# Performance work log

Hardware: AMD Instinct MI355X
Metric: run time of the kernel (lower is better)

## Reference

```python
import jax, jax.numpy as jnp
import numpy as np

NS, B, T, S, H, V, G = 30, 16, 8, 400, 400, 20000, 3


def setup_inputs() -> dict:
    key = jax.random.key(0)
    ks = jax.random.split(key, 16)
    f = lambda k, shp, s: jax.random.normal(k, shp, jnp.float32) * s
    return dict(
        encoded_hidden=f(ks[0], (B, H), 1.0),
        encoded_outputs=f(ks[1], (B, S, H), 1.0),
        slot_emb=f(ks[2], (NS, H), 0.1),
        emb=f(ks[3], (V, H), 0.1),
        W_ih=f(ks[4], (3 * H, H), 0.05),
        W_hh=f(ks[5], (3 * H, H), 0.05),
        b_ih=jnp.zeros((3 * H,), jnp.float32),
        b_hh=jnp.zeros((3 * H,), jnp.float32),
        W_ratio_w=f(ks[6], (1, 3 * H), 0.05),
        W_ratio_b=jnp.zeros((1,), jnp.float32),
        W_gate_w=f(ks[7], (G, H), 0.05),
        W_gate_b=jnp.zeros((G,), jnp.float32),
        story=jax.random.randint(ks[8], (B, S), 0, V),
        target=jax.random.randint(ks[9], (B, NS, T), 0, V),
        encoded_lens=jax.random.randint(ks[10], (B,), S // 2, S + 1).astype(jnp.int32),
    )


def reference(encoded_hidden, encoded_outputs, slot_emb, emb, W_ih, W_hh, b_ih, b_hh,
              W_ratio_w, W_ratio_b, W_gate_w, W_gate_b, story, target, encoded_lens):
    ns, h = slot_emb.shape
    b, s, _ = encoded_outputs.shape
    t = target.shape[2]
    v = emb.shape[0]
    bs = ns * b  # fused slot*batch decode rows (parallel_decode)

    enc_out = jnp.tile(encoded_outputs, (ns, 1, 1))            # [bs,S,H]
    story_r = jnp.tile(story, (ns, 1))                          # [bs,S]
    lens_r = jnp.tile(encoded_lens, (ns,))                      # [bs]
    mask = jnp.arange(s)[None, :] < lens_r[:, None]             # [bs,S]
    h0 = jnp.tile(encoded_hidden, (ns, 1))                      # [bs,H]
    x0 = jnp.broadcast_to(slot_emb[:, None, :], (ns, b, h)).reshape(bs, h)
    # teacher-forcing inputs, slot-major flatten like target[:, :, wi].T.flatten()
    tf_in = emb[jnp.transpose(target, (2, 1, 0)).reshape(t, bs)]  # [T,bs,H]
    row = jnp.arange(bs)[:, None]
    neg_inf = jnp.float32(-jnp.inf)

    def gru_cell(x, hid):
        gi = x @ W_ih.T + b_ih
        gh = hid @ W_hh.T + b_hh
        ir, iz, inn = jnp.split(gi, 3, axis=-1)
        hr, hz, hn = jnp.split(gh, 3, axis=-1)
        r = jax.nn.sigmoid(ir + hr)
        z = jax.nn.sigmoid(iz + hz)
        n = jnp.tanh(inn + r * hn)
        return (1.0 - z) * n + z * hid

    def step(carry, x_next):
        hid, x = carry
        h_new = gru_cell(x, hid)                                # dec_state == hidden for 1-step GRU
        scores = jnp.einsum('bh,bsh->bs', h_new, enc_out)
        scores = jnp.where(mask, scores, neg_inf)
        prob = jax.nn.softmax(scores, axis=1)
        context = jnp.einsum('bs,bsh->bh', prob, enc_out)
        p_vocab = jax.nn.softmax(h_new @ emb.T, axis=1)         # [bs,V]
        p_gen_vec = jnp.concatenate([h_new, context, x], axis=-1)
        switch = jax.nn.sigmoid(p_gen_vec @ W_ratio_w.T + W_ratio_b)  # [bs,1]
        p_ctx = jnp.zeros((bs, v), p_vocab.dtype).at[row, story_r].add(prob)
        final = (1.0 - switch) * p_ctx + switch * p_vocab
        gate = context @ W_gate_w.T + W_gate_b
        return (h_new, x_next), (final, gate)

    _, (finals, gates) = jax.lax.scan(step, (h0, x0), tf_in)
    all_point = finals.reshape(t, ns, b, v).transpose(1, 2, 0, 3)  # [NS,B,T,V]
    all_gate = gates[0].reshape(ns, b, -1)                          # gates from wi==0
    return all_point, all_gate
```

## Files before the change

kernel.cpp:

```cpp
#include <hip/hip_runtime.h>
#include <hip/hip_bf16.h>

#define NSLOT 30
#define BB    16
#define TT    8
#define SS    400
#define HH    400
#define KP    416
#define NKK   13
#define VV    20000
#define GG    3
#define BSR   480
#define NBN   157
#define NCT   1256
#define FRAG_STRIDE 512

typedef __attribute__((ext_vector_type(8))) short bf16x8;
typedef __attribute__((ext_vector_type(4))) float f32x4;

__device__ __forceinline__ short f2bfs(float f){
  __hip_bfloat16 h = __float2bfloat16(f);
  union { __hip_bfloat16 b; short u; } v; v.b = h; return v.u;
}
__device__ __forceinline__ float sigm(float x){ return 1.f / (1.f + __expf(-x)); }
__device__ __forceinline__ float tanh_fast(float x){
  float e = __expf(2.f * x);
  return 1.f - 2.f / (e + 1.f);
}
__device__ __forceinline__ float wred_max(float v){
  #pragma unroll
  for (int off = 32; off; off >>= 1) v = fmaxf(v, __shfl_xor(v, off, 64));
  return v;
}
__device__ __forceinline__ float wred_sum(float v){
  #pragma unroll
  for (int off = 32; off; off >>= 1) v += __shfl_xor(v, off, 64);
  return v;
}

__global__ __launch_bounds__(256) void k_init(const float* __restrict__ eh,
                                              const float* __restrict__ semb,
                                              float* __restrict__ h_ws,
                                              float* __restrict__ x_ws)
{
  int idx = blockIdx.x * 256 + threadIdx.x;
  if (idx >= BSR * HH) return;
  int r = idx / HH, k = idx - r * HH;
  int batch = r % BB, slot = r / BB;
  h_ws[idx] = eh[batch * HH + k];
  x_ws[idx] = semb[slot * HH + k];
}

__global__ __launch_bounds__(256) void k_cast_emb(const float* __restrict__ emb,
                                                  short* __restrict__ ebf)
{
  const int nunit = NCT * NKK * 64;
  for (int u = blockIdx.x * 256 + threadIdx.x; u < nunit; u += gridDim.x * 256){
    int lane = u & 63;
    int kt = u >> 6;
    int ctile = kt / NKK, kk = kt - ctile * NKK;
    int lg = lane >> 4, cl = lane & 15;
    int c = ctile * 16 + cl;
    int k = kk * 32 + lg * 8;
    bf16x8 o;
    if (c < VV && k < HH){
      const float* src = emb + (size_t)c * HH + k;
      #pragma unroll
      for (int j = 0; j < 8; ++j) o[j] = f2bfs(src[j]);
    } else {
      #pragma unroll
      for (int j = 0; j < 8; ++j) o[j] = 0;
    }
    *reinterpret_cast<bf16x8*>(ebf + (size_t)u * 8) = o;
  }
}

__device__ __forceinline__ void gemm_acc(const float* __restrict__ A,
                                         const float* __restrict__ W,
                                         int N, int v0, int row0, int t,
                                         float acc[4][4])
{
  __shared__ float Af[64][36];
  __shared__ float Bf[64][132];
  const int cidx = t & 31, ridx = t >> 5;
  const int c0 = cidx * 4, r0 = ridx * 4;

  for (int kc = 0; kc < HH; kc += 64){
    const int Kc = (HH - kc >= 64) ? 64 : (HH - kc);
    const int sh = (Kc == 64) ? 4 : 2;
    {
      const int nunit = 32 << sh;
      for (int u = t; u < nunit; u += 256){
        int r = u >> sh;
        int k = (u & ((1 << sh) - 1)) << 2;
        float4 a4 = *reinterpret_cast<const float4*>(A + (size_t)(row0 + r) * HH + kc + k);
        Af[k][r] = a4.x; Af[k+1][r] = a4.y; Af[k+2][r] = a4.z; Af[k+3][r] = a4.w;
      }
    }
    {
      const int nunit = 128 << sh;
      for (int u = t; u < nunit; u += 256){
        int c = u >> sh;
        int k = (u & ((1 << sh) - 1)) << 2;
        float f0 = 0.f, f1 = 0.f, f2 = 0.f, f3 = 0.f;
        int col = v0 + c;
        if (col < N){
          float4 e = *reinterpret_cast<const float4*>(W + (size_t)col * HH + kc + k);
          f0 = e.x; f1 = e.y; f2 = e.z; f3 = e.w;
        }
        Bf[k][c] = f0; Bf[k+1][c] = f1; Bf[k+2][c] = f2; Bf[k+3][c] = f3;
      }
    }
    __syncthreads();
    #pragma unroll 8
    for (int k = 0; k < Kc; ++k){
      float4 a = *reinterpret_cast<const float4*>(&Af[k][r0]);
      float4 b = *reinterpret_cast<const float4*>(&Bf[k][c0]);
      acc[0][0] += a.x*b.x; acc[0][1] += a.x*b.y; acc[0][2] += a.x*b.z; acc[0][3] += a.x*b.w;
      acc[1][0] += a.y*b.x; acc[1][1] += a.y*b.y; acc[1][2] += a.y*b.z; acc[1][3] += a.y*b.w;
      acc[2][0] += a.z*b.x; acc[2][1] += a.z*b.y; acc[2][2] += a.z*b.z; acc[2][3] += a.z*b.w;
      acc[3][0] += a.w*b.x; acc[3][1] += a.w*b.y; acc[3][2] += a.w*b.z; acc[3][3] += a.w*b.w;
    }
    __syncthreads();
  }
}

__global__ __launch_bounds__(256) void k_gemm2(const float* __restrict__ x,
                                               const float* __restrict__ h,
                                               const float* __restrict__ Wih,
                                               const float* __restrict__ Whh,
                                               float* __restrict__ gi,
                                               float* __restrict__ gh, int nb1)
{
  const float* A; const float* W; float* C;
  int bx = blockIdx.x;
  if (bx < nb1){ A = x; W = Wih; C = gi; }
  else         { A = h; W = Whh; C = gh; bx -= nb1; }
  const int N = 3 * HH, v0 = bx * 128, row0 = blockIdx.y * 32, t = threadIdx.x;
  float acc[4][4] = {{0.f}};
  gemm_acc(A, W, N, v0, row0, t, acc);
  const int c0 = (t & 31) * 4, r0 = (t >> 5) * 4;
  #pragma unroll
  for (int i = 0; i < 4; ++i){
    int rr = row0 + r0 + i;
    #pragma unroll
    for (int j = 0; j < 4; ++j){
      int col = v0 + c0 + j;
      if (col < N) C[(size_t)rr * N + col] = acc[i][j];
    }
  }
}

__global__ __launch_bounds__(256) void k_logits_mfma(
    const short* __restrict__ hbf, const short* __restrict__ ebf,
    float* __restrict__ out, float* __restrict__ pmax_ws,
    float* __restrict__ psum_ws, int wi)
{
  const int t = threadIdx.x;
  const int lane = t & 63, wid = t >> 6;
  const int wr = wid >> 1, wc = wid & 1;
  const int l15 = lane & 15, lg = lane >> 4;
  const int bM = blockIdx.x, bN = blockIdx.y;

  const short* ap[2];
  const short* bp[4];
  #pragma unroll
  for (int m = 0; m < 2; ++m){
    int rtile = bM * 4 + wr * 2 + m;
    ap[m] = hbf + (size_t)min(rtile, BSR / 16 - 1) * (NKK * FRAG_STRIDE) + lane * 8;
  }
  #pragma unroll
  for (int n = 0; n < 4; ++n){
    int ctile = bN * 8 + wc * 4 + n;
    bp[n] = ebf + (size_t)ctile * (NKK * FRAG_STRIDE) + lane * 8;
  }

  f32x4 acc[2][4];
  #pragma unroll
  for (int m = 0; m < 2; ++m)
    #pragma unroll
    for (int n = 0; n < 4; ++n)
      acc[m][n] = (f32x4){0.f, 0.f, 0.f, 0.f};

  #pragma unroll
  for (int kk = 0; kk < NKK; ++kk){
    const int ko = kk * FRAG_STRIDE;
    bf16x8 a0 = *reinterpret_cast<const bf16x8*>(ap[0] + ko);
    bf16x8 a1 = *reinterpret_cast<const bf16x8*>(ap[1] + ko);
    #pragma unroll
    for (int n = 0; n < 4; ++n){
      bf16x8 b = *reinterpret_cast<const bf16x8*>(bp[n] + ko);
      acc[0][n] = __builtin_amdgcn_mfma_f32_16x16x32_bf16(a0, b, acc[0][n], 0, 0, 0);
      acc[1][n] = __builtin_amdgcn_mfma_f32_16x16x32_bf16(a1, b, acc[1][n], 0, 0, 0);
    }
  }

  #pragma unroll
  for (int m = 0; m < 2; ++m){
    #pragma unroll
    for (int q = 0; q < 4; ++q){
      int row = bM * 64 + wr * 32 + m * 16 + lg * 4 + q;
      if (row < BSR){
        float* orow = out + ((size_t)row * TT + wi) * VV;
        #pragma unroll
        for (int n = 0; n < 4; ++n){
          int col = bN * 128 + wc * 64 + n * 16 + l15;
          if (col < VV) orow[col] = acc[m][n][q];
        }
      }
    }
    f32x4 rmax, rsum;
    #pragma unroll
    for (int q = 0; q < 4; ++q){
      float mx = -3.0e38f;
      #pragma unroll
      for (int n = 0; n < 4; ++n){
        int col = bN * 128 + wc * 64 + n * 16 + l15;
        float v = (col < VV) ? acc[m][n][q] : -3.0e38f;
        mx = fmaxf(mx, v);
      }
      #pragma unroll
      for (int off = 1; off < 16; off <<= 1) mx = fmaxf(mx, __shfl_xor(mx, off, 64));
      float sm = 0.f;
      #pragma unroll
      for (int n = 0; n < 4; ++n){
        int col = bN * 128 + wc * 64 + n * 16 + l15;
        if (col < VV) sm += __expf(acc[m][n][q] - mx);
      }
      #pragma unroll
      for (int off = 1; off < 16; off <<= 1) sm += __shfl_xor(sm, off, 64);
      rmax[q] = mx; rsum[q] = sm;
    }
    if (l15 == 0){
      #pragma unroll
      for (int q = 0; q < 4; ++q){
        int row = bM * 64 + wr * 32 + m * 16 + lg * 4 + q;
        if (row < BSR){
          size_t pidx = ((size_t)row * NBN + bN) * 2 + wc;
          pmax_ws[pidx] = rmax[q];
          psum_ws[pidx] = rsum[q];
        }
      }
    }
  }
}

__global__ __launch_bounds__(256) void k_att(
    const float* __restrict__ enc, const float* __restrict__ emb,
    const float* __restrict__ b_ih, const float* __restrict__ b_hh,
    const float* __restrict__ Wr_w, const float* __restrict__ Wr_b,
    const float* __restrict__ Wg_w, const float* __restrict__ Wg_b,
    const int* __restrict__ target, const int* __restrict__ lens,
    const float* __restrict__ gi_ws, const float* __restrict__ gh_ws,
    float* __restrict__ h_ws, float* __restrict__ x_ws,
    short* __restrict__ h_bf,
    float* __restrict__ prob_ws, float* __restrict__ sw_ws,
    float* __restrict__ d_out, int wi)
{
  __shared__ float hn_s[HH];
  __shared__ float sc_s[SS];
  __shared__ float ctx_s[HH];
  __shared__ float red[4];
  __shared__ float redg[GG][4];

  const int t = threadIdx.x;
  const int rg = blockIdx.x;
  const int batch = rg % BB, slot = rg / BB;
  const int len = lens[batch];

  const float* gir = gi_ws + (size_t)rg * (3 * HH);
  const float* ghr = gh_ws + (size_t)rg * (3 * HH);
  for (int k = t; k < HH; k += 256){
    float irv = gir[k]          + b_ih[k];
    float izv = gir[HH + k]     + b_ih[HH + k];
    float inv = gir[2 * HH + k] + b_ih[2 * HH + k];
    float hrv = ghr[k]          + b_hh[k];
    float hzv = ghr[HH + k]     + b_hh[HH + k];
    float hnv = ghr[2 * HH + k] + b_hh[2 * HH + k];
    float rr = sigm(irv + hrv);
    float zz = sigm(izv + hzv);
    float nn = tanh_fast(inv + rr * hnv);
    float hold = h_ws[(size_t)rg * HH + k];
    float hnew = (1.f - zz) * nn + zz * hold;
    hn_s[k] = hnew;
    h_ws[(size_t)rg * HH + k] = hnew;
  }
  __syncthreads();

  if (t < KP / 8){
    const int kk = t >> 2, lg = t & 3;
    const int rtile = rg >> 4, rl = rg & 15;
    bf16x8 o;
    #pragma unroll
    for (int j = 0; j < 8; ++j){
      int k = t * 8 + j;
      o[j] = (k < HH) ? f2bfs(hn_s[k]) : (short)0;
    }
    *reinterpret_cast<bf16x8*>(
        h_bf + ((size_t)rtile * NKK + kk) * FRAG_STRIDE + (lg * 16 + rl) * 8) = o;
  }

  const float* encb = enc + (size_t)batch * SS * HH;
  float lmax = -3.0e38f;
  for (int s = t; s < SS; s += 256){
    if (s < len){
      const float4* er4 = reinterpret_cast<const float4*>(encb + (size_t)s * HH);
      float dot = 0.f;
      for (int k4 = 0; k4 < HH / 4; ++k4){
        float4 e = er4[k4];
        float4 hv = *reinterpret_cast<const float4*>(&hn_s[k4 * 4]);
        dot += e.x*hv.x + e.y*hv.y + e.z*hv.z + e.w*hv.w;
      }
      sc_s[s] = dot;
      lmax = fmaxf(lmax, dot);
    }
  }
  lmax = wred_max(lmax);
  if ((t & 63) == 0) red[t >> 6] = lmax;
  __syncthreads();
  lmax = fmaxf(fmaxf(red[0], red[1]), fmaxf(red[2], red[3]));
  float lsum = 0.f;
  for (int s = t; s < SS; s += 256){
    float e = (s < len) ? __expf(sc_s[s] - lmax) : 0.f;
    sc_s[s] = e;
    lsum += e;
  }
  lsum = wred_sum(lsum);
  __syncthreads();
  if ((t & 63) == 0) red[t >> 6] = lsum;
  __syncthreads();
  lsum = red[0] + red[1] + red[2] + red[3];
  float invl = 1.f / lsum;
  for (int s = t; s < SS; s += 256){
    float p = sc_s[s] * invl;
    sc_s[s] = p;
    prob_ws[(size_t)rg * SS + s] = p;
  }
  __syncthreads();

  for (int k = t; k < HH; k += 256){
    float c = 0.f;
    for (int s = 0; s < len; ++s)
      c += sc_s[s] * encb[(size_t)s * HH + k];
    ctx_s[k] = c;
  }
  __syncthreads();

  float sa = 0.f;
  for (int k = t; k < HH; k += 256){
    sa += Wr_w[k]          * hn_s[k]
        + Wr_w[HH + k]     * ctx_s[k]
        + Wr_w[2 * HH + k] * x_ws[(size_t)rg * HH + k];
  }
  sa = wred_sum(sa);
  if ((t & 63) == 0) red[t >> 6] = sa;
  __syncthreads();
  sa = red[0] + red[1] + red[2] + red[3];
  if (t == 0) sw_ws[rg] = sigm(sa + Wr_b[0]);

  if (wi == 0){
    float ga[GG] = {0.f, 0.f, 0.f};
    for (int k = t; k < HH; k += 256){
      float cv = ctx_s[k];
      ga[0] += Wg_w[k] * cv;
      ga[1] += Wg_w[HH + k] * cv;
      ga[2] += Wg_w[2 * HH + k] * cv;
    }
    #pragma unroll
    for (int g = 0; g < GG; ++g){
      ga[g] = wred_sum(ga[g]);
      if ((t & 63) == 0) redg[g][t >> 6] = ga[g];
    }
    __syncthreads();
    if (t < GG)
      d_out[(size_t)NSLOT * BB * TT * VV + (size_t)rg * GG + t] =
          redg[t][0] + redg[t][1] + redg[t][2] + redg[t][3] + Wg_b[t];
  }

  const int tgt = target[batch * (NSLOT * TT) + slot * TT + wi];
  const float* embrow = emb + (size_t)tgt * HH;
  for (int k = t; k < HH; k += 256)
    x_ws[(size_t)rg * HH + k] = embrow[k];
}

__global__ __launch_bounds__(256) void k_finalize(
    float* __restrict__ logits_out, const float* __restrict__ prob_ws,
    const float* __restrict__ pmax_ws, const float* __restrict__ psum_ws,
    const float* __restrict__ sw_ws, const int* __restrict__ story,
    const int* __restrict__ lens, int wi)
{
  __shared__ float pctx[VV];
  __shared__ float red[4];
  const int t = threadIdx.x;
  const int r = blockIdx.x;
  const int batch = r % BB;
  for (int v = t; v < VV; v += 256) pctx[v] = 0.f;
  __syncthreads();
  const int len = lens[batch];
  for (int s = t; s < SS; s += 256){
    if (s < len)
      atomicAdd(&pctx[story[batch * SS + s]], prob_ws[(size_t)r * SS + s]);
  }

  const float* pm = pmax_ws + (size_t)r * (NBN * 2);
  const float* ps = psum_ws + (size_t)r * (NBN * 2);
  float m = -3.0e38f;
  for (int i = t; i < NBN * 2; i += 256) m = fmaxf(m, pm[i]);
  m = wred_max(m);
  if ((t & 63) == 0) red[t >> 6] = m;
  __syncthreads();
  m = fmaxf(fmaxf(red[0], red[1]), fmaxf(red[2], red[3]));
  float lsum = 0.f;
  for (int i = t; i < NBN * 2; i += 256) lsum += ps[i] * __expf(pm[i] - m);
  lsum = wred_sum(lsum);
  __syncthreads();
  if ((t & 63) == 0) red[t >> 6] = lsum;
  __syncthreads();
  lsum = red[0] + red[1] + red[2] + red[3];

  const float sw = sw_ws[r];
  const float invl = sw / lsum;
  const float osw = 1.f - sw;
  float* lrow = logits_out + ((size_t)r * TT + wi) * VV;
  const float4* l4 = reinterpret_cast<const float4*>(lrow);
  float4* o4 = reinterpret_cast<float4*>(lrow);
  for (int i = t; i < VV / 4; i += 256){
    float4 q = l4[i];
    int v = i * 4;
    float4 o;
    o.x = __expf(q.x - m) * invl + osw * pctx[v + 0];
    o.y = __expf(q.y - m) * invl + osw * pctx[v + 1];
    o.z = __expf(q.z - m) * invl + osw * pctx[v + 2];
    o.w = __expf(q.w - m) * invl + osw * pctx[v + 3];
    o4[i] = o;
  }
}

extern "C" void kernel_launch(void* const* d_in, const int* in_sizes, int n_in,
                              void* d_out, int out_size, void* d_ws, size_t ws_size,
                              hipStream_t stream)
{
  (void)in_sizes; (void)n_in; (void)out_size; (void)ws_size;
  const float* eh    = (const float*)d_in[0];
  const float* enc   = (const float*)d_in[1];
  const float* semb  = (const float*)d_in[2];
  const float* emb   = (const float*)d_in[3];
  const float* W_ih  = (const float*)d_in[4];
  const float* W_hh  = (const float*)d_in[5];
  const float* b_ih  = (const float*)d_in[6];
  const float* b_hh  = (const float*)d_in[7];
  const float* Wr_w  = (const float*)d_in[8];
  const float* Wr_b  = (const float*)d_in[9];
  const float* Wg_w  = (const float*)d_in[10];
  const float* Wg_b  = (const float*)d_in[11];
  const int* story = (const int*)d_in[12];
  const int* tgt   = (const int*)d_in[13];
  const int* lens  = (const int*)d_in[14];
  float* out = (float*)d_out;

  float* ws      = (float*)d_ws;
  float* h_ws    = ws;
  float* x_ws    = ws + 192000;
  float* prob_ws = ws + 384000;
  float* sw_ws   = ws + 576000;
  float* gi_ws   = ws + 576512;
  float* gh_ws   = ws + 1152512;
  float* pmax_ws = ws + 1728512;
  float* psum_ws = ws + 1879552;
  short* h_bf    = (short*)(ws + 2030592);
  short* emb_bf  = (short*)(ws + 2130432);

  k_cast_emb<<<2048, 256, 0, stream>>>(emb, emb_bf);
  k_init<<<750, 256, 0, stream>>>(eh, semb, h_ws, x_ws);
  for (int wi = 0; wi < TT; ++wi){
    dim3 gg(20, 15);
    k_gemm2<<<gg, 256, 0, stream>>>(x_ws, h_ws, W_ih, W_hh, gi_ws, gh_ws, 10);
    k_att<<<BSR, 256, 0, stream>>>(enc, emb, b_ih, b_hh, Wr_w, Wr_b, Wg_w, Wg_b,
                                   tgt, lens, gi_ws, gh_ws, h_ws, x_ws, h_bf,
                                   prob_ws, sw_ws, out, wi);
    dim3 gl(8, NBN);
    k_logits_mfma<<<gl, 256, 0, stream>>>(h_bf, emb_bf, out, pmax_ws, psum_ws, wi);
    k_finalize<<<BSR, 256, 0, stream>>>(out, prob_ws, pmax_ws, psum_ws,
                                        sw_ws, story, lens, wi);
  }
}
```

Baseline: 1.178 ms.

## Store logits as packed bf16 in output row and enlarge MFMA M tile

The logits kernel now writes bf16 logits packed two per 32-bit word into the first half of each output row, halving the logit write and the finalize read traffic. Finalize first copies the bf16 row into shared memory so it can then overwrite the same row in place with fp32 probabilities. Each logits block also now computes four 16-row M tiles per wave instead of two, halving the grid in M and reusing each B fragment across more MFMAs at the cost of more accumulator registers. Rounding logits to bf16 before the exp adds small numerical error to the vocabulary probabilities.

Result: faster. 1.144 ms (-2.9%).

```diff
diff --git a/kernel.cpp b/kernel.cpp
--- a/kernel.cpp
+++ b/kernel.cpp
@@ -15,12 +15,19 @@
 #define NCT   1256
 #define FRAG_STRIDE 512
 
+typedef unsigned short u16;
 typedef __attribute__((ext_vector_type(8))) short bf16x8;
 typedef __attribute__((ext_vector_type(4))) float f32x4;
 
 __device__ __forceinline__ short f2bfs(float f){
   __hip_bfloat16 h = __float2bfloat16(f);
   union { __hip_bfloat16 b; short u; } v; v.b = h; return v.u;
+}
+__device__ __forceinline__ unsigned int pack2(float lo, float hi){
+  return (unsigned int)(u16)f2bfs(lo) | ((unsigned int)(u16)f2bfs(hi) << 16);
+}
+__device__ __forceinline__ float bfu(u16 u){
+  union { unsigned int i; float f; } v; v.i = ((unsigned int)u) << 16; return v.f;
 }
 __device__ __forceinline__ float sigm(float x){ return 1.f / (1.f + __expf(-x)); }
 __device__ __forceinline__ float tanh_fast(float x){
@@ -162,11 +169,11 @@
   const int l15 = lane & 15, lg = lane >> 4;
   const int bM = blockIdx.x, bN = blockIdx.y;
 
-  const short* ap[2];
+  const short* ap[4];
   const short* bp[4];
   #pragma unroll
-  for (int m = 0; m < 2; ++m){
-    int rtile = bM * 4 + wr * 2 + m;
+  for (int m = 0; m < 4; ++m){
+    int rtile = bM * 8 + wr * 4 + m;
     ap[m] = hbf + (size_t)min(rtile, BSR / 16 - 1) * (NKK * FRAG_STRIDE) + lane * 8;
   }
   #pragma unroll
@@ -175,9 +182,9 @@
     bp[n] = ebf + (size_t)ctile * (NKK * FRAG_STRIDE) + lane * 8;
   }
 
-  f32x4 acc[2][4];
-  #pragma unroll
-  for (int m = 0; m < 2; ++m)
+  f32x4 acc[4][4];
+  #pragma unroll
+  for (int m = 0; m < 4; ++m)
     #pragma unroll
     for (int n = 0; n < 4; ++n)
       acc[m][n] = (f32x4){0.f, 0.f, 0.f, 0.f};
@@ -185,28 +192,32 @@
   #pragma unroll
   for (int kk = 0; kk < NKK; ++kk){
     const int ko = kk * FRAG_STRIDE;
-    bf16x8 a0 = *reinterpret_cast<const bf16x8*>(ap[0] + ko);
-    bf16x8 a1 = *reinterpret_cast<const bf16x8*>(ap[1] + ko);
+    bf16x8 a[4];
+    #pragma unroll
+    for (int m = 0; m < 4; ++m)
+      a[m] = *reinterpret_cast<const bf16x8*>(ap[m] + ko);
     #pragma unroll
     for (int n = 0; n < 4; ++n){
       bf16x8 b = *reinterpret_cast<const bf16x8*>(bp[n] + ko);
-      acc[0][n] = __builtin_amdgcn_mfma_f32_16x16x32_bf16(a0, b, acc[0][n], 0, 0, 0);
-      acc[1][n] = __builtin_amdgcn_mfma_f32_16x16x32_bf16(a1, b, acc[1][n], 0, 0, 0);
-    }
-  }
-
-  #pragma unroll
-  for (int m = 0; m < 2; ++m){
+      #pragma unroll
+      for (int m = 0; m < 4; ++m)
+        acc[m][n] = __builtin_amdgcn_mfma_f32_16x16x32_bf16(a[m], b, acc[m][n], 0, 0, 0);
+    }
+  }
+
+  #pragma unroll
+  for (int m = 0; m < 4; ++m){
     #pragma unroll
     for (int q = 0; q < 4; ++q){
-      int row = bM * 64 + wr * 32 + m * 16 + lg * 4 + q;
-      if (row < BSR){
-        float* orow = out + ((size_t)row * TT + wi) * VV;
-        #pragma unroll
-        for (int n = 0; n < 4; ++n){
-          int col = bN * 128 + wc * 64 + n * 16 + l15;
-          if (col < VV) orow[col] = acc[m][n][q];
-        }
+      int row = bM * 128 + wr * 64 + m * 16 + lg * 4 + q;
+      u16* lrow16 = reinterpret_cast<u16*>(out + ((size_t)row * TT + wi) * VV);
+      #pragma unroll
+      for (int n = 0; n < 4; ++n){
+        float v = acc[m][n][q];
+        float vp = __shfl_xor(v, 1, 64);
+        int col = bN * 128 + wc * 64 + n * 16 + l15;
+        if (((l15 & 1) == 0) && row < BSR && col < VV)
+          *reinterpret_cast<unsigned int*>(lrow16 + col) = pack2(v, vp);
       }
     }
     f32x4 rmax, rsum;
@@ -234,7 +245,7 @@
     if (l15 == 0){
       #pragma unroll
       for (int q = 0; q < 4; ++q){
-        int row = bM * 64 + wr * 32 + m * 16 + lg * 4 + q;
+        int row = bM * 128 + wr * 64 + m * 16 + lg * 4 + q;
         if (row < BSR){
           size_t pidx = ((size_t)row * NBN + bN) * 2 + wc;
           pmax_ws[pidx] = rmax[q];
@@ -390,6 +401,7 @@
     const int* __restrict__ lens, int wi)
 {
   __shared__ float pctx[VV];
+  __shared__ u16 rowbuf[VV];
   __shared__ float red[4];
   const int t = threadIdx.x;
   const int r = blockIdx.x;
@@ -401,6 +413,11 @@
     if (s < len)
       atomicAdd(&pctx[story[batch * SS + s]], prob_ws[(size_t)r * SS + s]);
   }
+
+  float* lrow = logits_out + ((size_t)r * TT + wi) * VV;
+  const uint4* l16 = reinterpret_cast<const uint4*>(lrow);
+  for (int i = t; i < VV / 8; i += 256)
+    reinterpret_cast<uint4*>(rowbuf)[i] = l16[i];
 
   const float* pm = pmax_ws + (size_t)r * (NBN * 2);
   const float* ps = psum_ws + (size_t)r * (NBN * 2);
@@ -421,17 +438,15 @@
   const float sw = sw_ws[r];
   const float invl = sw / lsum;
   const float osw = 1.f - sw;
-  float* lrow = logits_out + ((size_t)r * TT + wi) * VV;
-  const float4* l4 = reinterpret_cast<const float4*>(lrow);
   float4* o4 = reinterpret_cast<float4*>(lrow);
   for (int i = t; i < VV / 4; i += 256){
-    float4 q = l4[i];
+    ushort4 s4 = reinterpret_cast<const ushort4*>(rowbuf)[i];
     int v = i * 4;
     float4 o;
-    o.x = __expf(q.x - m) * invl + osw * pctx[v + 0];
-    o.y = __expf(q.y - m) * invl + osw * pctx[v + 1];
-    o.z = __expf(q.z - m) * invl + osw * pctx[v + 2];
-    o.w = __expf(q.w - m) * invl + osw * pctx[v + 3];
+    o.x = __expf(bfu(s4.x) - m) * invl + osw * pctx[v + 0];
+    o.y = __expf(bfu(s4.y) - m) * invl + osw * pctx[v + 1];
+    o.z = __expf(bfu(s4.z) - m) * invl + osw * pctx[v + 2];
+    o.w = __expf(bfu(s4.w) - m) * invl + osw * pctx[v + 3];
     o4[i] = o;
   }
 }
@@ -478,7 +493,7 @@
     k_att<<<BSR, 256, 0, stream>>>(enc, emb, b_ih, b_hh, Wr_w, Wr_b, Wg_w, Wg_b,
                                    tgt, lens, gi_ws, gh_ws, h_ws, x_ws, h_bf,
                                    prob_ws, sw_ws, out, wi);
-    dim3 gl(8, NBN);
+    dim3 gl(4, NBN);
     k_logits_mfma<<<gl, 256, 0, stream>>>(h_bf, emb_bf, out, pmax_ws, psum_ws, wi);
     k_finalize<<<BSR, 256, 0, stream>>>(out, prob_ws, pmax_ws, psum_ws,
                                         sw_ws, story, lens, wi);
```
